# Optimization experiments

Measured on AMD Instinct MI355X. Metric: run time of the kernel, lower is better.

Reference implementation:

```python
import jax, jax.numpy as jnp
import numpy as np

TIME = 4096
DIM = 2048
DT_TAU = 0.1 / 1.0  # dt / tau


def setup_inputs() -> dict:
    key = jax.random.key(0)
    k1, k2, k3, k4 = jax.random.split(key, 4)
    inputs = jax.random.normal(k1, (TIME, 1, DIM), dtype=jnp.float32)
    W = jax.random.normal(k2, (DIM, DIM), dtype=jnp.float32) * 0.02  # recurrent weight (nn.Linear, bias=False)
    bias = jax.random.normal(k3, (1, DIM), dtype=jnp.float32)
    initial = jax.random.normal(k4, (1, DIM), dtype=jnp.float32)
    return {"inputs": inputs, "W": W, "bias": bias, "initial": initial}


def reference(inputs, W, bias, initial):
    # states[0] = initial; states[t+1] = s*(1-dt/tau) + (dt/tau)*(sigmoid(s+bias)@W.T + inputs[t])
    def step(state, x_t):
        f = jax.nn.sigmoid(state + bias) @ W.T  # [1, dim]
        new_state = state * (1.0 - DT_TAU) + DT_TAU * (f + x_t)
        return new_state, new_state

    _, rest = jax.lax.scan(step, initial, inputs[: TIME - 1])  # rest: [time-1, 1, dim]
    return jnp.concatenate([initial[None], rest], axis=0)  # [time, 1, dim]
```

## Files before the change

### kernel.cpp

```cpp
#include <hip/hip_runtime.h>
#include <hip/hip_fp16.h>
#include <hip/hip_cooperative_groups.h>
#include <stdint.h>

#define TIME_STEPS 4096
#define DIM        2048
#define NBLK       256
#define NTH        512
#define NWORK      32
#define WVB        8
#define RPW        8

typedef uint32_t u32x4 __attribute__((ext_vector_type(4)));
typedef _Float16 h2f16 __attribute__((ext_vector_type(2)));


__device__ __forceinline__ uint32_t umin32(uint32_t a, uint32_t b) { return a < b ? a : b; }

__device__ __forceinline__ float dot2f(uint32_t packed, h2f16 w, float acc) {
#if __has_builtin(__builtin_amdgcn_fdot2)
  return __builtin_amdgcn_fdot2(__builtin_bit_cast(h2f16, packed), w, acc, false);
#else
  h2f16 a = __builtin_bit_cast(h2f16, packed);
  acc = fmaf((float)a.x, (float)w.x, acc);
  return fmaf((float)a.y, (float)w.y, acc);
#endif
}

__device__ __forceinline__ int swz(int p) { return p ^ (((p >> 5) & 7) << 2); }

template<int NSLOT>
__global__ __launch_bounds__(NTH, 2) void ctrnn_kernel(
    const float* __restrict__ x,
    const float* __restrict__ W,
    const float* __restrict__ bias,
    const float* __restrict__ initial,
    float* __restrict__ out,
    uint32_t* __restrict__ actbuf,
    uint32_t* __restrict__ progress,
    uint32_t* __restrict__ xccmap)
{
  const int tid  = threadIdx.x;
  const int lane = tid & 63;
  const int wv   = tid >> 6;

  if (tid == 0) {
    uint32_t xcc;
    asm volatile("s_getreg_b32 %0, hwreg(HW_REG_XCC_ID)" : "=s"(xcc));
    __hip_atomic_store(&xccmap[blockIdx.x], xcc,
                       __ATOMIC_RELAXED, __HIP_MEMORY_SCOPE_AGENT);
  }
  cooperative_groups::this_grid().sync();

  __shared__ uint32_t s_map[NBLK];
  for (int i = tid; i < NBLK; i += NTH)
    s_map[i] = __hip_atomic_load(&xccmap[i], __ATOMIC_RELAXED, __HIP_MEMORY_SCOPE_AGENT);
  __syncthreads();
  const uint32_t target = s_map[0];
  int before = 0, total = 0, beforeN = 0;
  const int bid = blockIdx.x;
  for (int i = 0; i < NBLK; ++i) {
    const bool m = (s_map[i] == target);
    total += m;
    if (i < bid) { before += m; beforeN += !m; }
  }
  const bool mine = (s_map[bid] == target);
  const int rank = mine ? before : (total + beforeN);
  if (rank >= NWORK) return;
  const int wb = rank;

  __shared__ uint32_t lds[2][1024];

  const int gwid = wb * WVB + wv;
  const int row0 = gwid * RPW;

  h2f16 w2[RPW][16];
  #pragma unroll
  for (int m = 0; m < RPW; ++m) {
    const float* wr = W + (size_t)(row0 + m) * DIM + lane * 32;
    #pragma unroll
    for (int q = 0; q < 16; ++q)
      w2[m][q] = h2f16{(_Float16)wr[2*q], (_Float16)wr[2*q+1]};
  }

  const int xq = lane >> 3, xr = lane & 7;
  float xa = x[(size_t)xq * DIM + row0 + xr];
  float xb = x[(size_t)(8 + xq) * DIM + row0 + xr];
  float xa2 = 0.f, xb2 = 0.f;
  int t0 = 0;

  float v = 0.f, bj = 0.f;
  if (lane < RPW) {
    const int j = row0 + lane;
    v  = initial[j];
    bj = bias[j];
    out[j] = v;
    const float a0 = 1.0f / (1.0f + __expf(-(v + bj)));
    __half h = __float2half_rn(a0);
    uint16_t hb; __builtin_memcpy(&hb, &h, 2);
    __hip_atomic_store(&actbuf[j], (1u << 16) | hb,
                       __ATOMIC_RELAXED, __HIP_MEMORY_SCOPE_AGENT);
  }

  const int e0 = wv * 256 + lane * 4;
  const int p0 = e0 >> 1;

  uint32_t prog_seen = 0;

  for (int t = 0; t < TIME_STEPS - 1; ++t) {
    const int b = t & 1;
    const int off = t - t0;
    const uint32_t needtag = (uint32_t)(t + 1);
    const uint32_t thresh  = needtag << 16;

    const uint32_t* qsrc = actbuf + (size_t)(t & (NSLOT - 1)) * DIM + e0;
    u32x4 q;
    bool ok = false;
    do {
      if (!ok) {
        asm volatile("global_load_dwordx4 %0, %1, off sc1\n\t"
                     "s_waitcnt vmcnt(0)"
                     : "=&v"(q) : "v"(qsrc) : "memory");
        ok = umin32(umin32(q[0], q[1]), umin32(q[2], q[3])) >= thresh;
      }
    } while (!__all((int)ok));

    {
      const uint32_t lo = __builtin_amdgcn_perm(q[1], q[0], 0x05040100u);
      const uint32_t hi = __builtin_amdgcn_perm(q[3], q[2], 0x05040100u);
      const int w0 = swz(p0);
      lds[b][w0]     = lo;
      lds[b][w0 + 1] = hi;
    }

    __syncthreads();

    if (tid == 0)
      __hip_atomic_store(&progress[wb], needtag,
                         __ATOMIC_RELAXED, __HIP_MEMORY_SCOPE_AGENT);

    if (off == 13) {
      const int ta = min(t0 + 16 + xq, TIME_STEPS - 1);
      const int tb = min(t0 + 24 + xq, TIME_STEPS - 1);
      xa2 = x[(size_t)ta * DIM + row0 + xr];
      xb2 = x[(size_t)tb * DIM + row0 + xr];
    }

    float a0 = 0.f, a1 = 0.f, a2 = 0.f, a3 = 0.f;
    float a4 = 0.f, a5 = 0.f, a6 = 0.f, a7 = 0.f;
    #pragma unroll
    for (int j = 0; j < 4; ++j) {
      const u32x4 qq = *reinterpret_cast<const u32x4*>(&lds[b][swz(lane * 16 + 4 * j)]);
      #pragma unroll
      for (int i = 0; i < 4; ++i) {
        const uint32_t pr = qq[i];
        const int idx = 4 * j + i;
        a0 = dot2f(pr, w2[0][idx], a0);
        a1 = dot2f(pr, w2[1][idx], a1);
        a2 = dot2f(pr, w2[2][idx], a2);
        a3 = dot2f(pr, w2[3][idx], a3);
        a4 = dot2f(pr, w2[4][idx], a4);
        a5 = dot2f(pr, w2[5][idx], a5);
        a6 = dot2f(pr, w2[6][idx], a6);
        a7 = dot2f(pr, w2[7][idx], a7);
      }
    }

    const float t0r = a0 + __shfl_xor(a0, 1, 64);
    const float t1r = a1 + __shfl_xor(a1, 1, 64);
    const float t2r = a2 + __shfl_xor(a2, 1, 64);
    const float t3r = a3 + __shfl_xor(a3, 1, 64);
    const float t4r = a4 + __shfl_xor(a4, 1, 64);
    const float t5r = a5 + __shfl_xor(a5, 1, 64);
    const float t6r = a6 + __shfl_xor(a6, 1, 64);
    const float t7r = a7 + __shfl_xor(a7, 1, 64);
    float b0 = (lane & 1) ? t1r : t0r;
    float b1 = (lane & 1) ? t3r : t2r;
    float b2 = (lane & 1) ? t5r : t4r;
    float b3 = (lane & 1) ? t7r : t6r;
    b0 += __shfl_xor(b0, 2, 64);
    b1 += __shfl_xor(b1, 2, 64);
    b2 += __shfl_xor(b2, 2, 64);
    b3 += __shfl_xor(b3, 2, 64);
    float c0 = (lane & 2) ? b1 : b0;
    float c1 = (lane & 2) ? b3 : b2;
    c0 += __shfl_xor(c0, 4, 64);
    c1 += __shfl_xor(c1, 4, 64);
    float p = (lane & 4) ? c1 : c0;
    p += __shfl_xor(p, 8, 64);
    p += __shfl_xor(p, 16, 64);
    p += __shfl_xor(p, 32, 64);

    if (t >= NSLOT - 1) {
      const uint32_t need = (uint32_t)(t + 2 - NSLOT);
      if (need > prog_seen) {
        for (;;) {
          uint32_t mn = __hip_atomic_load(&progress[lane & (NWORK - 1)],
                            __ATOMIC_RELAXED, __HIP_MEMORY_SCOPE_AGENT);
          uint32_t qv;
          qv = (uint32_t)__shfl_xor((int)mn, 1, 64);  mn = umin32(mn, qv);
          qv = (uint32_t)__shfl_xor((int)mn, 2, 64);  mn = umin32(mn, qv);
          qv = (uint32_t)__shfl_xor((int)mn, 4, 64);  mn = umin32(mn, qv);
          qv = (uint32_t)__shfl_xor((int)mn, 8, 64);  mn = umin32(mn, qv);
          qv = (uint32_t)__shfl_xor((int)mn, 16, 64); mn = umin32(mn, qv);
          if (mn >= need) { prog_seen = mn; break; }
          __builtin_amdgcn_s_sleep(1);
        }
      }
    }

    const float xsrc = (off < 8) ? xa : xb;
    const float xvt  = __shfl(xsrc, ((off & 7) << 3) | xr, 64);

    if (lane < RPW) {
      v = 0.9f * v + 0.1f * (p + xvt);
      const float a = 1.0f / (1.0f + __expf(-(v + bj)));
      __half h = __float2half_rn(a);
      uint16_t hb; __builtin_memcpy(&hb, &h, 2);
      const uint32_t e = ((uint32_t)(t + 2) << 16) | hb;
      __hip_atomic_store(&actbuf[(size_t)((t + 1) & (NSLOT - 1)) * DIM + row0 + lane], e,
                         __ATOMIC_RELAXED, __HIP_MEMORY_SCOPE_AGENT);
      out[(size_t)(t + 1) * DIM + row0 + lane] = v;
    }

    if (off == 15) { t0 += 16; xa = xa2; xb = xb2; }
  }
}

extern "C" void kernel_launch(void* const* d_in, const int* in_sizes, int n_in,
                              void* d_out, int out_size, void* d_ws, size_t ws_size,
                              hipStream_t stream) {
  const float* x       = (const float*)d_in[0];
  const float* W       = (const float*)d_in[1];
  const float* bias    = (const float*)d_in[2];
  const float* initial = (const float*)d_in[3];
  float* out           = (float*)d_out;

  uint32_t* actbuf = (uint32_t*)d_ws;

  const size_t need8 = ((size_t)8 * DIM + NWORK + NBLK) * 4;
  void* kfun;
  size_t ringwords;
  if (ws_size >= need8) { kfun = (void*)ctrnn_kernel<8>; ringwords = (size_t)8 * DIM; }
  else                  { kfun = (void*)ctrnn_kernel<2>; ringwords = (size_t)2 * DIM; }

  uint32_t* progress = actbuf + ringwords;
  uint32_t* xccmap   = progress + NWORK;

  hipMemsetAsync(d_ws, 0, (ringwords + NWORK + NBLK) * 4, stream);

  void* args[] = { (void*)&x, (void*)&W, (void*)&bias, (void*)&initial,
                   (void*)&out, (void*)&actbuf, (void*)&progress, (void*)&xccmap };
  hipLaunchCooperativeKernel(kfun, dim3(NBLK), dim3(NTH), args, 0, stream);
}
```

Measured before the change: 9.568 ms.

## Remap lanes to row/column-chunk layout and double-buffer activation polling loads

Each lane now holds weights for a single row over a 256-column chunk (lane&7 picks the row, lane>>3 the chunk) instead of 8 rows over 32 columns. The cross-lane reduction shrinks from a transpose-style shuffle tree to three xor shuffles, with the LDS swizzle adjusted to match. The spin-wait on the activation ring keeps two loads in flight so a fresh poll is already pending when a check fails. In exchange, each lane reads the same LDS broadcast pattern across 8 lanes, and the extra outstanding loads add memory traffic while waiting.

```diff
diff --git a/kernel.cpp b/kernel.cpp
--- a/kernel.cpp
+++ b/kernel.cpp
@@ -27,7 +27,11 @@
 #endif
 }
 
-__device__ __forceinline__ int swz(int p) { return p ^ (((p >> 5) & 7) << 2); }
+__device__ __forceinline__ int swz2(int p) { return p ^ (((p >> 7) & 7) << 2); }
+
+#define POLL_ISSUE(dst, src)                                       \
+  asm volatile("global_load_dwordx4 %0, %1, off sc1"               \
+               : "=&v"(dst) : "v"(src) : "memory")
 
 template<int NSLOT>
 __global__ __launch_bounds__(NTH, 2) void ctrnn_kernel(
@@ -74,13 +78,15 @@
   const int gwid = wb * WVB + wv;
   const int row0 = gwid * RPW;
 
-  h2f16 w2[RPW][16];
-  #pragma unroll
-  for (int m = 0; m < RPW; ++m) {
-    const float* wr = W + (size_t)(row0 + m) * DIM + lane * 32;
+  const int r_ = lane & 7;
+  const int c_ = lane >> 3;
+
+  h2f16 w2[128];
+  {
+    const float* wr = W + (size_t)(row0 + r_) * DIM + c_ * 256;
     #pragma unroll
-    for (int q = 0; q < 16; ++q)
-      w2[m][q] = h2f16{(_Float16)wr[2*q], (_Float16)wr[2*q+1]};
+    for (int q = 0; q < 128; ++q)
+      w2[q] = h2f16{(_Float16)wr[2*q], (_Float16)wr[2*q+1]};
   }
 
   const int xq = lane >> 3, xr = lane & 7;
@@ -114,21 +120,26 @@
     const uint32_t thresh  = needtag << 16;
 
     const uint32_t* qsrc = actbuf + (size_t)(t & (NSLOT - 1)) * DIM + e0;
-    u32x4 q;
-    bool ok = false;
-    do {
-      if (!ok) {
-        asm volatile("global_load_dwordx4 %0, %1, off sc1\n\t"
-                     "s_waitcnt vmcnt(0)"
-                     : "=&v"(q) : "v"(qsrc) : "memory");
-        ok = umin32(umin32(q[0], q[1]), umin32(q[2], q[3])) >= thresh;
-      }
-    } while (!__all((int)ok));
+    u32x4 qa, qb, q;
+    POLL_ISSUE(qa, qsrc);
+    POLL_ISSUE(qb, qsrc);
+    for (;;) {
+      asm volatile("s_waitcnt vmcnt(1)" ::: "memory");
+      __builtin_amdgcn_sched_barrier(0);
+      if (umin32(umin32(qa[0], qa[1]), umin32(qa[2], qa[3])) >= thresh) { q = qa; break; }
+      POLL_ISSUE(qa, qsrc);
+      asm volatile("s_waitcnt vmcnt(1)" ::: "memory");
+      __builtin_amdgcn_sched_barrier(0);
+      if (umin32(umin32(qb[0], qb[1]), umin32(qb[2], qb[3])) >= thresh) { q = qb; break; }
+      POLL_ISSUE(qb, qsrc);
+    }
+    asm volatile("s_waitcnt vmcnt(0)" ::: "memory");
+    __builtin_amdgcn_sched_barrier(0);
 
     {
       const uint32_t lo = __builtin_amdgcn_perm(q[1], q[0], 0x05040100u);
       const uint32_t hi = __builtin_amdgcn_perm(q[3], q[2], 0x05040100u);
-      const int w0 = swz(p0);
+      const int w0 = swz2(p0);
       lds[b][w0]     = lo;
       lds[b][w0 + 1] = hi;
     }
@@ -146,47 +157,17 @@
       xb2 = x[(size_t)tb * DIM + row0 + xr];
     }
 
-    float a0 = 0.f, a1 = 0.f, a2 = 0.f, a3 = 0.f;
-    float a4 = 0.f, a5 = 0.f, a6 = 0.f, a7 = 0.f;
+    float ac0 = 0.f, ac1 = 0.f, ac2 = 0.f, ac3 = 0.f;
+    const int cbase = c_ * 128;
     #pragma unroll
-    for (int j = 0; j < 4; ++j) {
-      const u32x4 qq = *reinterpret_cast<const u32x4*>(&lds[b][swz(lane * 16 + 4 * j)]);
-      #pragma unroll
-      for (int i = 0; i < 4; ++i) {
-        const uint32_t pr = qq[i];
-        const int idx = 4 * j + i;
-        a0 = dot2f(pr, w2[0][idx], a0);
-        a1 = dot2f(pr, w2[1][idx], a1);
-        a2 = dot2f(pr, w2[2][idx], a2);
-        a3 = dot2f(pr, w2[3][idx], a3);
-        a4 = dot2f(pr, w2[4][idx], a4);
-        a5 = dot2f(pr, w2[5][idx], a5);
-        a6 = dot2f(pr, w2[6][idx], a6);
-        a7 = dot2f(pr, w2[7][idx], a7);
-      }
-    }
-
-    const float t0r = a0 + __shfl_xor(a0, 1, 64);
-    const float t1r = a1 + __shfl_xor(a1, 1, 64);
-    const float t2r = a2 + __shfl_xor(a2, 1, 64);
-    const float t3r = a3 + __shfl_xor(a3, 1, 64);
-    const float t4r = a4 + __shfl_xor(a4, 1, 64);
-    const float t5r = a5 + __shfl_xor(a5, 1, 64);
-    const float t6r = a6 + __shfl_xor(a6, 1, 64);
-    const float t7r = a7 + __shfl_xor(a7, 1, 64);
-    float b0 = (lane & 1) ? t1r : t0r;
-    float b1 = (lane & 1) ? t3r : t2r;
-    float b2 = (lane & 1) ? t5r : t4r;
-    float b3 = (lane & 1) ? t7r : t6r;
-    b0 += __shfl_xor(b0, 2, 64);
-    b1 += __shfl_xor(b1, 2, 64);
-    b2 += __shfl_xor(b2, 2, 64);
-    b3 += __shfl_xor(b3, 2, 64);
-    float c0 = (lane & 2) ? b1 : b0;
-    float c1 = (lane & 2) ? b3 : b2;
-    c0 += __shfl_xor(c0, 4, 64);
-    c1 += __shfl_xor(c1, 4, 64);
-    float p = (lane & 4) ? c1 : c0;
+    for (int j = 0; j < 32; ++j) {
+      const u32x4 qq = *reinterpret_cast<const u32x4*>(&lds[b][swz2(cbase + 4 * j)]);
+      ac0 = dot2f(qq[0], w2[4*j+0], ac0);
+      ac1 = dot2f(qq[1], w2[4*j+1], ac1);
+      ac2 = dot2f(qq[2], w2[4*j+2], ac2);
+      ac3 = dot2f(qq[3], w2[4*j+3], ac3);
+    }
+    float p = (ac0 + ac1) + (ac2 + ac3);
     p += __shfl_xor(p, 8, 64);
     p += __shfl_xor(p, 16, 64);
     p += __shfl_xor(p, 32, 64);
```

Result: faster. 9.036 ms (-5.6%).
